# Kernel tuning notes

Measured on AMD Instinct MI355X. Metric: run time of the kernel, lower is better.

## Reference

```python
import jax, jax.numpy as jnp
import numpy as np
from jax import lax

B, T = 64, 200
NUM_C, DIM_S, SIZE_M = 2000, 128, 50


def setup_inputs() -> dict:
    key = jax.random.key(0)
    ks = jax.random.split(key, 12)
    d = {}
    d['skill'] = jax.random.randint(ks[0], (B, T), 0, NUM_C)
    d['answer'] = jax.random.randint(ks[1], (B, T), 0, 2)
    s = 1.0 / np.sqrt(DIM_S)
    d['k_emb'] = jax.random.normal(ks[2], (NUM_C + 1, DIM_S), jnp.float32)
    d['v_emb'] = jax.random.normal(ks[3], (2 * NUM_C + 1, DIM_S), jnp.float32)
    # kaiming_normal on [size_m, dim_s]: std = sqrt(2/dim_s)
    d['Mk'] = jax.random.normal(ks[4], (SIZE_M, DIM_S), jnp.float32) * np.sqrt(2.0 / DIM_S)
    d['Mv0'] = jax.random.normal(ks[5], (SIZE_M, DIM_S), jnp.float32) * np.sqrt(2.0 / DIM_S)
    d['f_W'] = jax.random.normal(ks[6], (DIM_S, 2 * DIM_S), jnp.float32) * (1.0 / np.sqrt(2 * DIM_S))
    d['f_b'] = jnp.zeros((DIM_S,), jnp.float32)
    d['p_W'] = jax.random.normal(ks[7], (NUM_C, DIM_S), jnp.float32) * s
    d['p_b'] = jnp.zeros((NUM_C,), jnp.float32)
    d['e_W'] = jax.random.normal(ks[8], (DIM_S, DIM_S), jnp.float32) * s
    d['e_b'] = jnp.zeros((DIM_S,), jnp.float32)
    d['a_W'] = jax.random.normal(ks[9], (DIM_S, DIM_S), jnp.float32) * s
    d['a_b'] = jnp.zeros((DIM_S,), jnp.float32)
    return d


def reference(skill, answer, k_emb, v_emb, Mk, Mv0, f_W, f_b, p_W, p_b, e_W, e_b, a_W, a_b):
    num_c = p_W.shape[0]
    bsz = skill.shape[0]
    answer_x = jnp.where(answer == 2, 1, answer)
    x = skill + num_c * answer_x                       # [B,T]
    k = k_emb[skill]                                   # [B,T,D]
    v = v_emb[x]                                       # [B,T,D]
    w = jax.nn.softmax(jnp.einsum('btd,md->btm', k, Mk), axis=-1)   # [B,T,M]
    e = jax.nn.sigmoid(jnp.einsum('btd,ed->bte', v, e_W) + e_b)      # [B,T,D]
    a = jnp.tanh(jnp.einsum('btd,ed->bte', v, a_W) + a_b)            # [B,T,D]

    Mv_init = jnp.broadcast_to(Mv0, (bsz,) + Mv0.shape)              # [B,M,D]

    def step(Mvt, inp):
        et, at, wt = inp                               # [B,D],[B,D],[B,M]
        # read uses pre-update memory (Mv[:, :-1] in the torch code)
        read = jnp.einsum('bm,bmd->bd', wt, Mvt)
        Mvt_new = Mvt * (1.0 - wt[:, :, None] * et[:, None, :]) + wt[:, :, None] * at[:, None, :]
        return Mvt_new, read

    _, reads = lax.scan(step, Mv_init,
                        (e.transpose(1, 0, 2), a.transpose(1, 0, 2), w.transpose(1, 0, 2)))
    reads = reads.transpose(1, 0, 2)                   # [B,T,D]

    f = jnp.tanh(jnp.concatenate([reads, k], axis=-1) @ f_W.T + f_b)  # [B,T,D]
    p = jax.nn.sigmoid(f @ p_W.T + p_b)                # [B,T,num_c] (dropout is identity at eval)
    p = p[:, :-1, :]
    next_skill = skill[:, 1:]                          # [B,T-1]
    idx = jnp.minimum(next_skill, num_c - 1)
    pred = jnp.take_along_axis(p, idx[..., None], axis=-1)[..., 0]
    pred = jnp.where(next_skill < num_c, pred, 0.0)    # index num_c -> zero row in torch one_hot
    return pred
```

## Files before the change

kernel.cpp:

```cpp
#include <hip/hip_runtime.h>
#include <math.h>

#define Bsz 64
#define Tn 200
#define NUMC 2000
#define DS 128
#define SM 50
#define NTOK (Bsz*Tn)
#define WG 5
#define MPG 10

typedef __attribute__((ext_vector_type(8))) short bfrag;
typedef __attribute__((ext_vector_type(4))) float f32x4;
typedef __attribute__((ext_vector_type(4))) unsigned int u32x4;

__device__ __forceinline__ unsigned short f2bf(float x) {
    unsigned int u = __builtin_bit_cast(unsigned int, x);
    u = u + 0x7fffu + ((u >> 16) & 1u);
    return (unsigned short)(u >> 16);
}
__device__ __forceinline__ unsigned int pack2(float a, float b) {
    return (unsigned int)f2bf(a) | ((unsigned int)f2bf(b) << 16);
}
__device__ __forceinline__ bfrag mk_frag(f32x4 x, f32x4 y) {
    u32x4 t;
    t[0] = pack2(x[0], x[1]); t[1] = pack2(x[2], x[3]);
    t[2] = pack2(y[0], y[1]); t[3] = pack2(y[2], y[3]);
    return __builtin_bit_cast(bfrag, t);
}

__global__ __launch_bounds__(256) void k0_cast(
    const float* __restrict__ eW, const float* __restrict__ aW,
    const float* __restrict__ fW, const float* __restrict__ Mk,
    unsigned int* __restrict__ BeaU, unsigned int* __restrict__ BkmU,
    unsigned int* __restrict__ Bf0U)
{
    const int g = blockIdx.x * 256 + threadIdx.x;
    if (g >= 9216) return;
    int gm, mat;
    unsigned int* dst;
    if (g < 4096)      { mat = 0; gm = g;        dst = BeaU; }
    else if (g < 7168) { mat = 1; gm = g - 4096; dst = BkmU; }
    else               { mat = 2; gm = g - 7168; dst = Bf0U; }
    const int nt = gm >> 8, r = gm & 255, ki = r >> 6, L = r & 63;
    const int n = nt * 16 + (L & 15);
    const int k = ki * 32 + (L >> 4) * 8;

    const float* src = nullptr;
    if (mat == 0) {
        src = (n < 128) ? (eW + (size_t)n * DS + k) : (aW + (size_t)(n - 128) * DS + k);
    } else if (mat == 1) {
        if (n < 128)      src = fW + (size_t)n * (2 * DS) + DS + k;
        else if (n < 128 + SM) src = Mk + (size_t)(n - 128) * DS + k;
    } else {
        src = fW + (size_t)n * (2 * DS) + k;
    }
    float v[8];
    #pragma unroll
    for (int j = 0; j < 8; j++) v[j] = src ? src[j] : 0.f;
    u32x4 o;
    o[0] = pack2(v[0], v[1]); o[1] = pack2(v[2], v[3]);
    o[2] = pack2(v[4], v[5]); o[3] = pack2(v[6], v[7]);
    ((u32x4*)dst)[gm] = o;
}

__global__ __launch_bounds__(256) void k1_gemm(
    const int* __restrict__ skill, const int* __restrict__ answer,
    const float* __restrict__ k_emb, const float* __restrict__ v_emb,
    const unsigned int* __restrict__ BeaU, const unsigned int* __restrict__ BkmU,
    const float* __restrict__ eB, const float* __restrict__ aB,
    float* __restrict__ w_buf, float* __restrict__ e_buf,
    float* __restrict__ a_buf, float* __restrict__ kp_buf)
{
    const int tid = threadIdx.x;
    const int w = tid >> 6, L = tid & 63, L15 = L & 15, quad = L >> 4;
    const int tok0 = blockIdx.x * 64;
    const int tokA = tok0 + 16 * w + L15;
    const int tokD0 = tok0 + 16 * w + quad * 4;

    const int s  = skill[tokA];
    const int an = answer[tokA];
    const int ax = (an == 2) ? 1 : an;
    const float* vp = v_emb + ((size_t)(s + NUMC * ax)) * DS + quad * 8;
    const float* kp = k_emb + (size_t)s * DS + quad * 8;

    bfrag Vf[4], Kf[4];
    #pragma unroll
    for (int ki = 0; ki < 4; ki++) {
        const f32x4* a = (const f32x4*)(vp + ki * 32);
        Vf[ki] = mk_frag(a[0], a[1]);
        const f32x4* b = (const f32x4*)(kp + ki * 32);
        Kf[ki] = mk_frag(b[0], b[1]);
    }

    const bfrag* Bea = (const bfrag*)BeaU;
    const bfrag* Bkm = (const bfrag*)BkmU;

    __shared__ float wl[64][52];

    for (int nt0 = 0; nt0 < 16; nt0 += 4) {
        bfrag bf[4][4];
        #pragma unroll
        for (int t = 0; t < 4; t++)
            #pragma unroll
            for (int ki = 0; ki < 4; ki++)
                bf[t][ki] = Bea[(size_t)((nt0 + t) * 4 + ki) * 64 + L];
        f32x4 acc[4];
        #pragma unroll
        for (int t = 0; t < 4; t++) acc[t] = (f32x4){0.f, 0.f, 0.f, 0.f};
        #pragma unroll
        for (int ki = 0; ki < 4; ki++)
            #pragma unroll
            for (int t = 0; t < 4; t++)
                acc[t] = __builtin_amdgcn_mfma_f32_16x16x32_bf16(Vf[ki], bf[t][ki], acc[t], 0, 0, 0);
        #pragma unroll
        for (int t = 0; t < 4; t++) {
            const int n = (nt0 + t) * 16 + L15;
            if (n < 128) {
                const float bias = eB[n];
                #pragma unroll
                for (int reg = 0; reg < 4; reg++) {
                    const int tok = tokD0 + reg;
                    e_buf[(size_t)tok * DS + n] = 1.f / (1.f + expf(-(acc[t][reg] + bias)));
                }
            } else {
                const float bias = aB[n - 128];
                #pragma unroll
                for (int reg = 0; reg < 4; reg++) {
                    const int tok = tokD0 + reg;
                    a_buf[(size_t)tok * DS + (n - 128)] = tanhf(acc[t][reg] + bias);
                }
            }
        }
    }

    for (int nt0 = 0; nt0 < 12; nt0 += 4) {
        bfrag bf[4][4];
        #pragma unroll
        for (int t = 0; t < 4; t++)
            #pragma unroll
            for (int ki = 0; ki < 4; ki++)
                bf[t][ki] = Bkm[(size_t)((nt0 + t) * 4 + ki) * 64 + L];
        f32x4 acc[4];
        #pragma unroll
        for (int t = 0; t < 4; t++) acc[t] = (f32x4){0.f, 0.f, 0.f, 0.f};
        #pragma unroll
        for (int ki = 0; ki < 4; ki++)
            #pragma unroll
            for (int t = 0; t < 4; t++)
                acc[t] = __builtin_amdgcn_mfma_f32_16x16x32_bf16(Kf[ki], bf[t][ki], acc[t], 0, 0, 0);
        #pragma unroll
        for (int t = 0; t < 4; t++) {
            const int n = (nt0 + t) * 16 + L15;
            if (n < 128) {
                #pragma unroll
                for (int reg = 0; reg < 4; reg++) {
                    const int tok = tokD0 + reg;
                    kp_buf[(size_t)tok * DS + n] = acc[t][reg];
                }
            } else {
                const int c = n - 128;
                if (c < SM) {
                    #pragma unroll
                    for (int reg = 0; reg < 4; reg++)
                        wl[16 * w + quad * 4 + reg][c] = acc[t][reg];
                }
            }
        }
    }
    __syncthreads();
    if (tid < 64) {
        float mx = -1e30f;
        for (int m = 0; m < SM; m++) mx = fmaxf(mx, wl[tid][m]);
        float sum = 0.f;
        float ex[SM];
        for (int m = 0; m < SM; m++) { ex[m] = expf(wl[tid][m] - mx); sum += ex[m]; }
        const float inv = 1.f / sum;
        float* wp = w_buf + (size_t)(tok0 + tid) * SM;
        for (int m = 0; m < SM; m++) wp[m] = ex[m] * inv;
    }
}

__global__ __launch_bounds__(64) void k2_scan(
    const float* __restrict__ w_buf, const float* __restrict__ e_buf,
    const float* __restrict__ a_buf, const float* __restrict__ Mv0,
    float* __restrict__ part_buf)
{
    const int bi   = blockIdx.x;
    const int b    = bi / (2*WG);
    const int r    = bi % (2*WG);
    const int dh   = r / WG;
    const int mg   = r % WG;
    const int lane = threadIdx.x;
    const int d    = dh*64 + lane;
    const int m0   = mg * MPG;
    const int base = b * Tn;

    float Mv[MPG];
    #pragma unroll
    for (int m = 0; m < MPG; m++) Mv[m] = Mv0[(size_t)(m0+m)*DS + d];

    float* pout = part_buf + (size_t)mg * NTOK * DS;

    float ev0[4], av0[4], wv0[4][MPG];
    #pragma unroll
    for (int q = 0; q < 4; q++) {
        const int tf = base + q;
        ev0[q] = e_buf[(size_t)tf*DS + d];
        av0[q] = a_buf[(size_t)tf*DS + d];
        #pragma unroll
        for (int m = 0; m < MPG; m++) wv0[q][m] = w_buf[(size_t)tf*SM + m0 + m];
    }

    for (int tb = 0; tb < Tn; tb += 4) {
        float ev1[4] = {}, av1[4] = {}, wv1[4][MPG] = {};
        if (tb + 4 < Tn) {
            #pragma unroll
            for (int q = 0; q < 4; q++) {
                const int tf = base + tb + 4 + q;
                ev1[q] = e_buf[(size_t)tf*DS + d];
                av1[q] = a_buf[(size_t)tf*DS + d];
                #pragma unroll
                for (int m = 0; m < MPG; m++) wv1[q][m] = w_buf[(size_t)tf*SM + m0 + m];
            }
        }
        #pragma unroll
        for (int q = 0; q < 4; q++) {
            float rd = 0.f;
            #pragma unroll
            for (int m = 0; m < MPG; m++) {
                const float wm = wv0[q][m];
                rd = fmaf(wm, Mv[m], rd);
                Mv[m] = fmaf(-wm, fmaf(ev0[q], Mv[m], -av0[q]), Mv[m]);
            }
            pout[(size_t)(base + tb + q)*DS + d] = rd;
        }
        #pragma unroll
        for (int q = 0; q < 4; q++) {
            ev0[q] = ev1[q]; av0[q] = av1[q];
            #pragma unroll
            for (int m = 0; m < MPG; m++) wv0[q][m] = wv1[q][m];
        }
    }
}

__global__ __launch_bounds__(256) void k3_gemm(
    const float* __restrict__ part_buf, const float* __restrict__ kp_buf,
    const unsigned int* __restrict__ Bf0U, const float* __restrict__ fB,
    const float* __restrict__ pW, const float* __restrict__ pB,
    const int* __restrict__ skill, float* __restrict__ out)
{
    const int tid = threadIdx.x;
    const int w = tid >> 6, L = tid & 63, L15 = L & 15, quad = L >> 4;
    const int tok0 = blockIdx.x * 64;
    const int tokA = tok0 + 16 * w + L15;
    const int tokD0 = tok0 + 16 * w + quad * 4;

    bfrag Rf[4];
    #pragma unroll
    for (int ki = 0; ki < 4; ki++) {
        const float* p0 = part_buf + (size_t)tokA * DS + ki * 32 + quad * 8;
        f32x4 x = (f32x4){0.f,0.f,0.f,0.f}, y = (f32x4){0.f,0.f,0.f,0.f};
        #pragma unroll
        for (int g = 0; g < WG; g++) {
            const f32x4* q = (const f32x4*)(p0 + (size_t)g * NTOK * DS);
            x = x + q[0]; y = y + q[1];
        }
        Rf[ki] = mk_frag(x, y);
    }

    const bfrag* Bf0 = (const bfrag*)Bf0U;
    float f[4][8];

    for (int nt0 = 0; nt0 < 8; nt0 += 4) {
        bfrag bf[4][4];
        #pragma unroll
        for (int t = 0; t < 4; t++)
            #pragma unroll
            for (int ki = 0; ki < 4; ki++)
                bf[t][ki] = Bf0[(size_t)((nt0 + t) * 4 + ki) * 64 + L];
        f32x4 acc[4];
        #pragma unroll
        for (int t = 0; t < 4; t++) acc[t] = (f32x4){0.f, 0.f, 0.f, 0.f};
        #pragma unroll
        for (int ki = 0; ki < 4; ki++)
            #pragma unroll
            for (int t = 0; t < 4; t++)
                acc[t] = __builtin_amdgcn_mfma_f32_16x16x32_bf16(Rf[ki], bf[t][ki], acc[t], 0, 0, 0);
        #pragma unroll
        for (int t = 0; t < 4; t++) {
            const int n = (nt0 + t) * 16 + L15;
            const float fb = fB[n];
            #pragma unroll
            for (int reg = 0; reg < 4; reg++) {
                const int tok = tokD0 + reg;
                f[reg][nt0 + t] = tanhf(acc[t][reg] + kp_buf[(size_t)tok * DS + n] + fb);
            }
        }
    }

    #pragma unroll
    for (int reg = 0; reg < 4; reg++) {
        const int tok = tokD0 + reg;
        const int t = tok % Tn;
        const bool act = (t < Tn - 1);
        int sn = 0, ix = 0;
        float contrib = 0.f;
        if (act) {
            sn = skill[tok + 1];
            ix = (sn < NUMC) ? sn : (NUMC - 1);
            const float* pr = pW + (size_t)ix * DS + L15;
            #pragma unroll
            for (int nt = 0; nt < 8; nt++)
                contrib = fmaf(f[reg][nt], pr[nt * 16], contrib);
        }
        #pragma unroll
        for (int msk = 1; msk <= 8; msk <<= 1)
            contrib += __shfl_xor(contrib, msk);
        if (act && L15 == 0) {
            const float val = contrib + pB[ix];
            const float prd = (sn < NUMC) ? (1.f / (1.f + expf(-val))) : 0.f;
            out[(size_t)(tok / Tn) * (Tn - 1) + t] = prd;
        }
    }
}

extern "C" void kernel_launch(void* const* d_in, const int* in_sizes, int n_in,
                              void* d_out, int out_size, void* d_ws, size_t ws_size,
                              hipStream_t stream)
{
    const int*   skill  = (const int*)  d_in[0];
    const int*   answer = (const int*)  d_in[1];
    const float* k_emb  = (const float*)d_in[2];
    const float* v_emb  = (const float*)d_in[3];
    const float* Mk     = (const float*)d_in[4];
    const float* Mv0    = (const float*)d_in[5];
    const float* f_W    = (const float*)d_in[6];
    const float* f_b    = (const float*)d_in[7];
    const float* p_W    = (const float*)d_in[8];
    const float* p_b    = (const float*)d_in[9];
    const float* e_W    = (const float*)d_in[10];
    const float* e_b    = (const float*)d_in[11];
    const float* a_W    = (const float*)d_in[12];
    const float* a_b    = (const float*)d_in[13];
    float* out = (float*)d_out;

    float* ws       = (float*)d_ws;
    float* w_buf    = ws;
    float* e_buf    = w_buf    + (size_t)NTOK*SM;
    float* a_buf    = e_buf    + (size_t)NTOK*DS;
    float* kp_buf   = a_buf    + (size_t)NTOK*DS;
    float* part_buf = kp_buf   + (size_t)NTOK*DS;
    unsigned int* BeaU = (unsigned int*)(part_buf + (size_t)WG*NTOK*DS);
    unsigned int* BkmU = BeaU + 4096 * 4;
    unsigned int* Bf0U = BkmU + 3072 * 4;

    k0_cast<<<36, 256, 0, stream>>>(e_W, a_W, f_W, Mk, BeaU, BkmU, Bf0U);
    k1_gemm<<<NTOK/64, 256, 0, stream>>>(skill, answer, k_emb, v_emb,
        BeaU, BkmU, e_b, a_b, w_buf, e_buf, a_buf, kp_buf);
    k2_scan<<<Bsz*2*WG, 64, 0, stream>>>(w_buf, e_buf, a_buf, Mv0, part_buf);
    k3_gemm<<<NTOK/64, 256, 0, stream>>>(part_buf, kp_buf, Bf0U, f_b,
        p_W, p_b, skill, out);
}
```

Before: 165.8 us.

## Double-buffer weight fragments in GEMMs and deepen scan prefetch with finer memory split

The GEMM kernels now load the next group of B fragments before running the current MFMA group and its epilogue, so global loads overlap compute. The scan kernel splits the memory slots into 10 groups of 5 instead of 5 of 10, launching twice as many blocks with a shorter serial chain per step. It also uses a 4-stage ring of 2-step prefetches in place of the single 4-step double buffer. The trade-offs are doubled partial-sum traffic and reduction work in k3, plus higher register pressure from the buffered fragments.

```diff
diff --git a/kernel.cpp b/kernel.cpp
--- a/kernel.cpp
+++ b/kernel.cpp
@@ -7,8 +7,8 @@
 #define DS 128
 #define SM 50
 #define NTOK (Bsz*Tn)
-#define WG 5
-#define MPG 10
+#define WG2 10
+#define MPG2 5
 
 typedef __attribute__((ext_vector_type(8))) short bfrag;
 typedef __attribute__((ext_vector_type(4))) float f32x4;
@@ -27,6 +27,21 @@
     t[0] = pack2(x[0], x[1]); t[1] = pack2(x[2], x[3]);
     t[2] = pack2(y[0], y[1]); t[3] = pack2(y[2], y[3]);
     return __builtin_bit_cast(bfrag, t);
+}
+
+__device__ __forceinline__ void load_group(const bfrag* __restrict__ B, int nt0, int L, bfrag bf[4][4]) {
+    #pragma unroll
+    for (int t = 0; t < 4; t++)
+        #pragma unroll
+        for (int ki = 0; ki < 4; ki++)
+            bf[t][ki] = B[(size_t)((nt0 + t) * 4 + ki) * 64 + L];
+}
+__device__ __forceinline__ void mfma_group(const bfrag A[4], const bfrag bf[4][4], f32x4 acc[4]) {
+    #pragma unroll
+    for (int ki = 0; ki < 4; ki++)
+        #pragma unroll
+        for (int t = 0; t < 4; t++)
+            acc[t] = __builtin_amdgcn_mfma_f32_16x16x32_bf16(A[ki], bf[t][ki], acc[t], 0, 0, 0);
 }
 
 __global__ __launch_bounds__(256) void k0_cast(
@@ -98,73 +113,95 @@
 
     __shared__ float wl[64][52];
 
-    for (int nt0 = 0; nt0 < 16; nt0 += 4) {
-        bfrag bf[4][4];
-        #pragma unroll
-        for (int t = 0; t < 4; t++)
+    {
+        bfrag bfA[4][4], bfB[4][4];
+        load_group(Bea, 0, L, bfA);
+        load_group(Bea, 4, L, bfB);
+
+        #define EA_EPI_E(NT0, ACC)                                              \
+            { _Pragma("unroll")                                                 \
+              for (int t = 0; t < 4; t++) {                                     \
+                const int n = (NT0 + t) * 16 + L15;                             \
+                const float bias = eB[n];                                       \
+                _Pragma("unroll")                                               \
+                for (int reg = 0; reg < 4; reg++)                               \
+                    e_buf[(size_t)(tokD0 + reg) * DS + n] =                     \
+                        1.f / (1.f + expf(-(ACC[t][reg] + bias)));              \
+              } }
+        #define EA_EPI_A(NT0, ACC)                                              \
+            { _Pragma("unroll")                                                 \
+              for (int t = 0; t < 4; t++) {                                     \
+                const int n = (NT0 + t) * 16 + L15 - 128;                       \
+                const float bias = aB[n];                                       \
+                _Pragma("unroll")                                               \
+                for (int reg = 0; reg < 4; reg++)                               \
+                    a_buf[(size_t)(tokD0 + reg) * DS + n] =                     \
+                        tanhf(ACC[t][reg] + bias);                              \
+              } }
+
+        f32x4 acc[4];
+        #pragma unroll
+        for (int t = 0; t < 4; t++) acc[t] = (f32x4){0.f,0.f,0.f,0.f};
+        mfma_group(Vf, bfA, acc);
+        load_group(Bea, 8, L, bfA);
+        EA_EPI_E(0, acc);
+
+        #pragma unroll
+        for (int t = 0; t < 4; t++) acc[t] = (f32x4){0.f,0.f,0.f,0.f};
+        mfma_group(Vf, bfB, acc);
+        load_group(Bea, 12, L, bfB);
+        EA_EPI_E(4, acc);
+
+        #pragma unroll
+        for (int t = 0; t < 4; t++) acc[t] = (f32x4){0.f,0.f,0.f,0.f};
+        mfma_group(Vf, bfA, acc);
+        EA_EPI_A(8, acc);
+
+        #pragma unroll
+        for (int t = 0; t < 4; t++) acc[t] = (f32x4){0.f,0.f,0.f,0.f};
+        mfma_group(Vf, bfB, acc);
+        EA_EPI_A(12, acc);
+    }
+
+    {
+        bfrag bfA[4][4], bfB[4][4];
+        load_group(Bkm, 0, L, bfA);
+        load_group(Bkm, 4, L, bfB);
+
+        f32x4 acc[4];
+        #pragma unroll
+        for (int t = 0; t < 4; t++) acc[t] = (f32x4){0.f,0.f,0.f,0.f};
+        mfma_group(Kf, bfA, acc);
+        load_group(Bkm, 8, L, bfA);
+        #pragma unroll
+        for (int t = 0; t < 4; t++) {
+            const int n = t * 16 + L15;
             #pragma unroll
-            for (int ki = 0; ki < 4; ki++)
-                bf[t][ki] = Bea[(size_t)((nt0 + t) * 4 + ki) * 64 + L];
-        f32x4 acc[4];
-        #pragma unroll
-        for (int t = 0; t < 4; t++) acc[t] = (f32x4){0.f, 0.f, 0.f, 0.f};
-        #pragma unroll
-        for (int ki = 0; ki < 4; ki++)
+            for (int reg = 0; reg < 4; reg++)
+                kp_buf[(size_t)(tokD0 + reg) * DS + n] = acc[t][reg];
+        }
+
+        #pragma unroll
+        for (int t = 0; t < 4; t++) acc[t] = (f32x4){0.f,0.f,0.f,0.f};
+        mfma_group(Kf, bfB, acc);
+        #pragma unroll
+        for (int t = 0; t < 4; t++) {
+            const int n = (4 + t) * 16 + L15;
             #pragma unroll
-            for (int t = 0; t < 4; t++)
-                acc[t] = __builtin_amdgcn_mfma_f32_16x16x32_bf16(Vf[ki], bf[t][ki], acc[t], 0, 0, 0);
+            for (int reg = 0; reg < 4; reg++)
+                kp_buf[(size_t)(tokD0 + reg) * DS + n] = acc[t][reg];
+        }
+
+        #pragma unroll
+        for (int t = 0; t < 4; t++) acc[t] = (f32x4){0.f,0.f,0.f,0.f};
+        mfma_group(Kf, bfA, acc);
         #pragma unroll
         for (int t = 0; t < 4; t++) {
-            const int n = (nt0 + t) * 16 + L15;
-            if (n < 128) {
-                const float bias = eB[n];
+            const int c = (8 + t) * 16 + L15 - 128;
+            if (c < SM) {
                 #pragma unroll
-                for (int reg = 0; reg < 4; reg++) {
-                    const int tok = tokD0 + reg;
-                    e_buf[(size_t)tok * DS + n] = 1.f / (1.f + expf(-(acc[t][reg] + bias)));
-                }
-            } else {
-                const float bias = aB[n - 128];
-                #pragma unroll
-                for (int reg = 0; reg < 4; reg++) {
-                    const int tok = tokD0 + reg;
-                    a_buf[(size_t)tok * DS + (n - 128)] = tanhf(acc[t][reg] + bias);
-                }
-            }
-        }
-    }
-
-    for (int nt0 = 0; nt0 < 12; nt0 += 4) {
-        bfrag bf[4][4];
-        #pragma unroll
-        for (int t = 0; t < 4; t++)
-            #pragma unroll
-            for (int ki = 0; ki < 4; ki++)
-                bf[t][ki] = Bkm[(size_t)((nt0 + t) * 4 + ki) * 64 + L];
-        f32x4 acc[4];
-        #pragma unroll
-        for (int t = 0; t < 4; t++) acc[t] = (f32x4){0.f, 0.f, 0.f, 0.f};
-        #pragma unroll
-        for (int ki = 0; ki < 4; ki++)
-            #pragma unroll
-            for (int t = 0; t < 4; t++)
-                acc[t] = __builtin_amdgcn_mfma_f32_16x16x32_bf16(Kf[ki], bf[t][ki], acc[t], 0, 0, 0);
-        #pragma unroll
-        for (int t = 0; t < 4; t++) {
-            const int n = (nt0 + t) * 16 + L15;
-            if (n < 128) {
-                #pragma unroll
-                for (int reg = 0; reg < 4; reg++) {
-                    const int tok = tokD0 + reg;
-                    kp_buf[(size_t)tok * DS + n] = acc[t][reg];
-                }
-            } else {
-                const int c = n - 128;
-                if (c < SM) {
-                    #pragma unroll
-                    for (int reg = 0; reg < 4; reg++)
-                        wl[16 * w + quad * 4 + reg][c] = acc[t][reg];
-                }
+                for (int reg = 0; reg < 4; reg++)
+                    wl[16 * w + quad * 4 + reg][c] = acc[t][reg];
             }
         }
     }
@@ -187,59 +224,55 @@
     float* __restrict__ part_buf)
 {
     const int bi   = blockIdx.x;
-    const int b    = bi / (2*WG);
-    const int r    = bi % (2*WG);
-    const int dh   = r / WG;
-    const int mg   = r % WG;
+    const int b    = bi / (2*WG2);
+    const int r    = bi % (2*WG2);
+    const int dh   = r / WG2;
+    const int mg   = r % WG2;
     const int lane = threadIdx.x;
     const int d    = dh*64 + lane;
-    const int m0   = mg * MPG;
+    const int m0   = mg * MPG2;
     const int base = b * Tn;
 
-    float Mv[MPG];
-    #pragma unroll
-    for (int m = 0; m < MPG; m++) Mv[m] = Mv0[(size_t)(m0+m)*DS + d];
+    float Mv[MPG2];
+    #pragma unroll
+    for (int m = 0; m < MPG2; m++) Mv[m] = Mv0[(size_t)(m0+m)*DS + d];
 
     float* pout = part_buf + (size_t)mg * NTOK * DS;
 
-    float ev0[4], av0[4], wv0[4][MPG];
-    #pragma unroll
-    for (int q = 0; q < 4; q++) {
-        const int tf = base + q;
-        ev0[q] = e_buf[(size_t)tf*DS + d];
-        av0[q] = a_buf[(size_t)tf*DS + d];
-        #pragma unroll
-        for (int m = 0; m < MPG; m++) wv0[q][m] = w_buf[(size_t)tf*SM + m0 + m];
-    }
-
-    for (int tb = 0; tb < Tn; tb += 4) {
-        float ev1[4] = {}, av1[4] = {}, wv1[4][MPG] = {};
-        if (tb + 4 < Tn) {
+    float se[4][2], sa[4][2], sw[4][2][MPG2];
+
+    #define LOADST(ST, T)                                                      \
+        { const int tc_ = ((T) < Tn) ? (T) : 0;                                \
+          _Pragma("unroll")                                                    \
+          for (int q_ = 0; q_ < 2; q_++) {                                     \
+              const int tf_ = base + tc_ + q_;                                 \
+              se[ST][q_] = e_buf[(size_t)tf_*DS + d];                          \
+              sa[ST][q_] = a_buf[(size_t)tf_*DS + d];                          \
+              _Pragma("unroll")                                                \
+              for (int m_ = 0; m_ < MPG2; m_++)                                \
+                  sw[ST][q_][m_] = w_buf[(size_t)tf_*SM + m0 + m_];            \
+          } }
+
+    LOADST(0, 0) LOADST(1, 2) LOADST(2, 4) LOADST(3, 6)
+
+    for (int i = 0; i < 25; i++) {
+        const int tb = i * 8;
+        #pragma unroll
+        for (int sub = 0; sub < 4; sub++) {
+            const int t0 = tb + sub * 2;
             #pragma unroll
-            for (int q = 0; q < 4; q++) {
-                const int tf = base + tb + 4 + q;
-                ev1[q] = e_buf[(size_t)tf*DS + d];
-                av1[q] = a_buf[(size_t)tf*DS + d];
+            for (int q = 0; q < 2; q++) {
+                const float ev = se[sub][q], av = sa[sub][q];
+                float rd = 0.f;
                 #pragma unroll
-                for (int m = 0; m < MPG; m++) wv1[q][m] = w_buf[(size_t)tf*SM + m0 + m];
+                for (int m = 0; m < MPG2; m++) {
+                    const float wm = sw[sub][q][m];
+                    rd = fmaf(wm, Mv[m], rd);
+                    Mv[m] = fmaf(-wm, fmaf(ev, Mv[m], -av), Mv[m]);
+                }
+                pout[(size_t)(base + t0 + q)*DS + d] = rd;
             }
-        }
-        #pragma unroll
-        for (int q = 0; q < 4; q++) {
-            float rd = 0.f;
-            #pragma unroll
-            for (int m = 0; m < MPG; m++) {
-                const float wm = wv0[q][m];
-                rd = fmaf(wm, Mv[m], rd);
-                Mv[m] = fmaf(-wm, fmaf(ev0[q], Mv[m], -av0[q]), Mv[m]);
-            }
-            pout[(size_t)(base + tb + q)*DS + d] = rd;
-        }
-        #pragma unroll
-        for (int q = 0; q < 4; q++) {
-            ev0[q] = ev1[q]; av0[q] = av1[q];
-            #pragma unroll
-            for (int m = 0; m < MPG; m++) wv0[q][m] = wv1[q][m];
+            LOADST(sub, t0 + 8)
         }
     }
 }
@@ -256,47 +289,49 @@
     const int tokA = tok0 + 16 * w + L15;
     const int tokD0 = tok0 + 16 * w + quad * 4;
 
+    const bfrag* Bf0 = (const bfrag*)Bf0U;
+    bfrag bfA[4][4], bfB[4][4];
+    load_group(Bf0, 0, L, bfA);
+    load_group(Bf0, 4, L, bfB);
+
     bfrag Rf[4];
     #pragma unroll
     for (int ki = 0; ki < 4; ki++) {
         const float* p0 = part_buf + (size_t)tokA * DS + ki * 32 + quad * 8;
         f32x4 x = (f32x4){0.f,0.f,0.f,0.f}, y = (f32x4){0.f,0.f,0.f,0.f};
         #pragma unroll
-        for (int g = 0; g < WG; g++) {
-            const f32x4* q = (const f32x4*)(p0 + (size_t)g * NTOK * DS);
-            x = x + q[0]; y = y + q[1];
+        for (int g = 0; g < WG2; g++) {
+            const f32x4* q4 = (const f32x4*)(p0 + (size_t)g * NTOK * DS);
+            x = x + q4[0]; y = y + q4[1];
         }
         Rf[ki] = mk_frag(x, y);
     }
 
-    const bfrag* Bf0 = (const bfrag*)Bf0U;
     float f[4][8];
-
-    for (int nt0 = 0; nt0 < 8; nt0 += 4) {
-        bfrag bf[4][4];
-        #pragma unroll
-        for (int t = 0; t < 4; t++)
-            #pragma unroll
-            for (int ki = 0; ki < 4; ki++)
-                bf[t][ki] = Bf0[(size_t)((nt0 + t) * 4 + ki) * 64 + L];
-        f32x4 acc[4];
-        #pragma unroll
-        for (int t = 0; t < 4; t++) acc[t] = (f32x4){0.f, 0.f, 0.f, 0.f};
-        #pragma unroll
-        for (int ki = 0; ki < 4; ki++)
-            #pragma unroll
-            for (int t = 0; t < 4; t++)
-                acc[t] = __builtin_amdgcn_mfma_f32_16x16x32_bf16(Rf[ki], bf[t][ki], acc[t], 0, 0, 0);
-        #pragma unroll
-        for (int t = 0; t < 4; t++) {
-            const int n = (nt0 + t) * 16 + L15;
-            const float fb = fB[n];
-            #pragma unroll
-            for (int reg = 0; reg < 4; reg++) {
-                const int tok = tokD0 + reg;
-                f[reg][nt0 + t] = tanhf(acc[t][reg] + kp_buf[(size_t)tok * DS + n] + fb);
-            }
-        }
+    f32x4 acc[4];
+
+    #pragma unroll
+    for (int t = 0; t < 4; t++) acc[t] = (f32x4){0.f,0.f,0.f,0.f};
+    mfma_group(Rf, bfA, acc);
+    #pragma unroll
+    for (int t = 0; t < 4; t++) {
+        const int n = t * 16 + L15;
+        const float fb = fB[n];
+        #pragma unroll
+        for (int reg = 0; reg < 4; reg++)
+            f[reg][t] = tanhf(acc[t][reg] + kp_buf[(size_t)(tokD0 + reg) * DS + n] + fb);
+    }
+
+    #pragma unroll
+    for (int t = 0; t < 4; t++) acc[t] = (f32x4){0.f,0.f,0.f,0.f};
+    mfma_group(Rf, bfB, acc);
+    #pragma unroll
+    for (int t = 0; t < 4; t++) {
+        const int n = (4 + t) * 16 + L15;
+        const float fb = fB[n];
+        #pragma unroll
+        for (int reg = 0; reg < 4; reg++)
+            f[reg][4 + t] = tanhf(acc[t][reg] + kp_buf[(size_t)(tokD0 + reg) * DS + n] + fb);
     }
 
     #pragma unroll
@@ -351,14 +386,14 @@
     float* a_buf    = e_buf    + (size_t)NTOK*DS;
     float* kp_buf   = a_buf    + (size_t)NTOK*DS;
     float* part_buf = kp_buf   + (size_t)NTOK*DS;
-    unsigned int* BeaU = (unsigned int*)(part_buf + (size_t)WG*NTOK*DS);
+    unsigned int* BeaU = (unsigned int*)(part_buf + (size_t)WG2*NTOK*DS);
     unsigned int* BkmU = BeaU + 4096 * 4;
     unsigned int* Bf0U = BkmU + 3072 * 4;
 
     k0_cast<<<36, 256, 0, stream>>>(e_W, a_W, f_W, Mk, BeaU, BkmU, Bf0U);
     k1_gemm<<<NTOK/64, 256, 0, stream>>>(skill, answer, k_emb, v_emb,
         BeaU, BkmU, e_b, a_b, w_buf, e_buf, a_buf, kp_buf);
-    k2_scan<<<Bsz*2*WG, 64, 0, stream>>>(w_buf, e_buf, a_buf, Mv0, part_buf);
+    k2_scan<<<Bsz*2*WG2, 64, 0, stream>>>(w_buf, e_buf, a_buf, Mv0, part_buf);
     k3_gemm<<<NTOK/64, 256, 0, stream>>>(part_buf, kp_buf, Bf0U, f_b,
         p_W, p_b, skill, out);
 }
```

New measurement: 156.5 us. 5.6% less time.
